# Kernel tuning notes

Measured on AMD Instinct MI355X. Metric: run time of the kernel, lower is better.

## Reference

```python
import jax, jax.numpy as jnp
import numpy as np
import math

D_MODEL = 1024
H = 16
D_K = D_MODEL // H
D_FF = 4096
NEG = -1e9


def layer_norm(x, alpha, bias):
    # Faithful to source: mean over last dim, UNBIASED std (torch.std default),
    # eps defined in source but never used in forward.
    mean = jnp.mean(x, axis=-1, keepdims=True)
    std = jnp.std(x, axis=-1, ddof=1, keepdims=True)
    return (x - mean) / std * alpha + bias


def mha(x, mask, w_q, w_k, w_v, w_o):
    B, S, D = x.shape
    q = (x @ w_q.T).reshape(B, S, H, D_K)
    k = (x @ w_k.T).reshape(B, S, H, D_K)
    v = (x @ w_v.T).reshape(B, S, H, D_K)
    scores = jnp.einsum('bqhd,bkhd->bhqk', q, k) / math.sqrt(D_K)
    scores = jnp.where(mask, NEG, scores)
    attn = jax.nn.softmax(scores, axis=-1)
    out = jnp.einsum('bhqk,bkhd->bqhd', attn, v).reshape(B, S, D)
    return out @ w_o.T


def setup_inputs() -> dict:
    key = jax.random.key(0)
    ks = jax.random.split(key, 16)
    B, S = 4, 2048
    s = 0.02
    return {
        'x': jax.random.normal(ks[0], (B, S, D_MODEL), jnp.float32),
        'w_q': jax.random.normal(ks[1], (D_MODEL, D_MODEL), jnp.float32) * s,
        'w_k': jax.random.normal(ks[2], (D_MODEL, D_MODEL), jnp.float32) * s,
        'w_v': jax.random.normal(ks[3], (D_MODEL, D_MODEL), jnp.float32) * s,
        'w_o': jax.random.normal(ks[4], (D_MODEL, D_MODEL), jnp.float32) * s,
        'l1_w': jax.random.normal(ks[5], (D_FF, D_MODEL), jnp.float32) * s,
        'l1_b': jnp.zeros((D_FF,), jnp.float32),
        'l2_w': jax.random.normal(ks[6], (D_MODEL, D_FF), jnp.float32) * s,
        'l2_b': jnp.zeros((D_MODEL,), jnp.float32),
        'norm1_a': jnp.ones((D_MODEL,), jnp.float32),
        'norm1_b': jnp.zeros((D_MODEL,), jnp.float32),
        'norm2_a': jnp.ones((D_MODEL,), jnp.float32),
        'norm2_b': jnp.zeros((D_MODEL,), jnp.float32),
        'normf_a': jnp.ones((D_MODEL,), jnp.float32),
        'normf_b': jnp.zeros((D_MODEL,), jnp.float32),
        'mask': jax.random.randint(ks[7], (B, 1, 1, S), 0, 2) == 1,
    }


def reference(x, w_q, w_k, w_v, w_o, l1_w, l1_b, l2_w, l2_b,
              norm1_a, norm1_b, norm2_a, norm2_b, normf_a, normf_b, mask):
    # residual 1: pre-norm self-attention (dropout is identity at eval)
    x = x + mha(layer_norm(x, norm1_a, norm1_b), mask, w_q, w_k, w_v, w_o)
    # residual 2: pre-norm FFN
    h = layer_norm(x, norm2_a, norm2_b)
    ff = jax.nn.relu(h @ l1_w.T + l1_b) @ l2_w.T + l2_b
    x = x + ff
    return layer_norm(x, normf_a, normf_b)
```

## Files before the change

kernel.cpp:

```cpp
#include <hip/hip_runtime.h>
#include <hip/hip_bf16.h>


typedef __bf16 bf16x8 __attribute__((ext_vector_type(8)));
typedef float f32x4 __attribute__((ext_vector_type(4)));
typedef unsigned short u16x8 __attribute__((ext_vector_type(8)));
using bf16 = __hip_bfloat16;

__device__ __forceinline__ f32x4 mfma16(bf16x8 a, bf16x8 b, f32x4 c) {
  return __builtin_amdgcn_mfma_f32_16x16x32_bf16(a, b, c, 0, 0, 0);
}

__device__ __forceinline__ int swz(int row, int blk) {
  return row * 64 + ((blk ^ (row & 7)) << 3);
}

__device__ __forceinline__ void stage_tile64(unsigned short* lds,
                                             const bf16* g, int ld, int rows) {
  const int lane = threadIdx.x & 63, wid = threadIdx.x >> 6;
  const int r8 = lane >> 3, blk = lane & 7;
  const bf16* gl = g + (size_t)r8 * ld + ((blk ^ r8) << 3);
  const int passes = rows >> 3;
  for (int p = wid; p < passes; p += 4) {
    __builtin_amdgcn_global_load_lds(
        (const __attribute__((address_space(1))) void*)(gl + (size_t)(p * 8) * ld),
        (__attribute__((address_space(3))) void*)(lds + p * 512),
        16, 0, 0);
  }
}

__device__ __forceinline__ short bfb(float x) {
  return (short)__hip_bfloat16_raw(__float2bfloat16(x)).x;
}

__global__ __launch_bounds__(256) void cvt_k(const float* __restrict__ s,
                                             bf16* __restrict__ d, int n) {
  const int i = (blockIdx.x * 256 + threadIdx.x) * 4;
  if (i + 3 < n) {
    const float4 v = *reinterpret_cast<const float4*>(s + i);
    ushort4 o;
    o.x = (unsigned short)bfb(v.x);
    o.y = (unsigned short)bfb(v.y);
    o.z = (unsigned short)bfb(v.z);
    o.w = (unsigned short)bfb(v.w);
    *reinterpret_cast<ushort4*>(d + i) = o;
  }
}

template <bool OUT_F32>
__global__ __launch_bounds__(256) void layernorm_k(const float* __restrict__ in,
                                                   const float* __restrict__ gamma,
                                                   const float* __restrict__ beta,
                                                   void* __restrict__ out) {
  __shared__ float red[8];
  const int row = blockIdx.x, t = threadIdx.x;
  const float4 vv = reinterpret_cast<const float4*>(in + (size_t)row * 1024)[t];
  const float x0 = vv.x, x1 = vv.y, x2 = vv.z, x3 = vv.w;
  float s = x0 + x1 + x2 + x3;
#pragma unroll
  for (int off = 32; off; off >>= 1) s += __shfl_down(s, off);
  if ((t & 63) == 0) red[t >> 6] = s;
  __syncthreads();
  const float mean = (red[0] + red[1] + red[2] + red[3]) * (1.0f / 1024.0f);
  const float d0 = x0 - mean, d1 = x1 - mean, d2 = x2 - mean, d3 = x3 - mean;
  float sq = d0 * d0 + d1 * d1 + d2 * d2 + d3 * d3;
#pragma unroll
  for (int off = 32; off; off >>= 1) sq += __shfl_down(sq, off);
  if ((t & 63) == 0) red[4 + (t >> 6)] = sq;
  __syncthreads();
  const float var =
      fmaxf((red[4] + red[5] + red[6] + red[7]) * (1.0f / 1023.0f), 1e-20f);
  const float rstd = rsqrtf(var);
  const float4 ga = reinterpret_cast<const float4*>(gamma)[t];
  const float4 be = reinterpret_cast<const float4*>(beta)[t];
  const float y0 = d0 * rstd * ga.x + be.x;
  const float y1 = d1 * rstd * ga.y + be.y;
  const float y2 = d2 * rstd * ga.z + be.z;
  const float y3 = d3 * rstd * ga.w + be.w;
  if (OUT_F32) {
    reinterpret_cast<float4*>((float*)out + (size_t)row * 1024)[t] =
        make_float4(y0, y1, y2, y3);
  } else {
    ushort4 o;
    o.x = (unsigned short)bfb(y0);
    o.y = (unsigned short)bfb(y1);
    o.z = (unsigned short)bfb(y2);
    o.w = (unsigned short)bfb(y3);
    reinterpret_cast<ushort4*>((bf16*)out + (size_t)row * 1024)[t] = o;
  }
}

template <bool HAS_BIAS, bool RELU, bool HAS_RES, bool OUT_F32, bool KV_EXIT>
__global__ __launch_bounds__(256) void gemm_bt(const bf16* __restrict__ A,
                                               const bf16* __restrict__ W,
                                               const float* __restrict__ bias,
                                               const float* __restrict__ resid,
                                               void* __restrict__ out,
                                               int M, int N, int K,
                                               int lda, int ldw,
                                               const int* __restrict__ cnt) {
  __shared__ __align__(16) unsigned short As[128 * 64];
  __shared__ __align__(16) unsigned short Bs[128 * 64];
  int bx = blockIdx.x, by = blockIdx.y;
  const int nwg = gridDim.x * gridDim.y;
  if ((nwg & 7) == 0) {
    const int lid = by * gridDim.x + bx;
    const int cpx = nwg >> 3;
    const int s = (lid & 7) * cpx + (lid >> 3);
    bx = s % gridDim.x;
    by = s / gridDim.x;
  }
  const int tm = bx * 128, tn = by * 128;
  if (KV_EXIT) {
    const int npad = (cnt[tm >> 11] + 127) & ~127;
    if ((tm & 2047) >= npad) return;
  }
  const int lane = threadIdx.x & 63, wid = threadIdx.x >> 6;
  const int n16 = lane & 15, quad = lane >> 4;
  const int wm = (wid >> 1) * 64, wn = (wid & 1) * 64;
  f32x4 acc[4][4] = {};
  for (int k0 = 0; k0 < K; k0 += 64) {
    stage_tile64(As, A + (size_t)tm * lda + k0, lda, 128);
    stage_tile64(Bs, W + (size_t)tn * ldw + k0, ldw, 128);
    __syncthreads();
#pragma unroll
    for (int kk = 0; kk < 64; kk += 32) {
      bf16x8 af[4], bw[4];
#pragma unroll
      for (int i = 0; i < 4; ++i)
        af[i] = *reinterpret_cast<const bf16x8*>(
            &As[swz(wm + i * 16 + n16, (kk >> 3) + quad)]);
#pragma unroll
      for (int j = 0; j < 4; ++j)
        bw[j] = *reinterpret_cast<const bf16x8*>(
            &Bs[swz(wn + j * 16 + n16, (kk >> 3) + quad)]);
#pragma unroll
      for (int i = 0; i < 4; ++i)
#pragma unroll
        for (int j = 0; j < 4; ++j) acc[i][j] = mfma16(af[i], bw[j], acc[i][j]);
    }
    __syncthreads();
  }
#pragma unroll
  for (int i = 0; i < 4; ++i) {
#pragma unroll
    for (int j = 0; j < 4; ++j) {
      const int n = tn + wn + j * 16 + n16;
      const float bv = HAS_BIAS ? bias[n] : 0.0f;
#pragma unroll
      for (int r = 0; r < 4; ++r) {
        const int m = tm + wm + i * 16 + quad * 4 + r;
        float vv = acc[i][j][r] + bv;
        if (RELU) vv = fmaxf(vv, 0.0f);
        if (HAS_RES) vv += resid[(size_t)m * N + n];
        if (OUT_F32)
          ((float*)out)[(size_t)m * N + n] = vv;
        else
          ((bf16*)out)[(size_t)m * N + n] = __float2bfloat16(vv);
      }
    }
  }
}

__global__ __launch_bounds__(256) void prep_mask_k(const int* __restrict__ m,
                                                   float* __restrict__ mf,
                                                   int n) {
  __shared__ int s;
  if (threadIdx.x == 0) s = 0;
  __syncthreads();
  unsigned int acc = 0;
  for (int i = threadIdx.x; i < 512; i += 256)
    acc |= ((const unsigned int*)m)[i] & 0xFFFFFF00u;
  if (acc) atomicOr(&s, 1);
  __syncthreads();
  const bool bytes = (s != 0);
  const int i = blockIdx.x * 256 + threadIdx.x;
  if (i < n) {
    const int v = bytes ? (int)((const unsigned char*)m)[i] : m[i];
    mf[i] = v ? -1.4427e9f : 0.0f;
  }
}

__global__ __launch_bounds__(256) void scan_k(const float* __restrict__ maskf,
                                              float* __restrict__ cmask,
                                              int* __restrict__ idx,
                                              int* __restrict__ cnt) {
  __shared__ int wsum[4];
  const int b = blockIdx.x, t = threadIdx.x, lane = t & 63, w = t >> 6;
  const float* mrow = maskf + b * 2048;
  int keep[8], local = 0;
#pragma unroll
  for (int e = 0; e < 8; ++e) {
    keep[e] = (mrow[t * 8 + e] == 0.0f) ? 1 : 0;
    local += keep[e];
  }
  int inc = local;
#pragma unroll
  for (int off = 1; off < 64; off <<= 1) {
    int v = __shfl_up(inc, off);
    if (lane >= off) inc += v;
  }
  if (lane == 63) wsum[w] = inc;
  __syncthreads();
  int base = 0;
#pragma unroll
  for (int i = 0; i < 4; ++i)
    if (i < w) base += wsum[i];
  int p = base + inc - local;
#pragma unroll
  for (int e = 0; e < 8; ++e)
    if (keep[e]) idx[b * 2048 + p++] = t * 8 + e;
  const int total = wsum[0] + wsum[1] + wsum[2] + wsum[3];
  if (t == 0) cnt[b] = total;
  for (int i = t; i < 2048; i += 256)
    cmask[b * 2048 + i] = (i < total) ? 0.0f : -1.4427e9f;
}

__global__ __launch_bounds__(128) void gatherA_k(const bf16* __restrict__ ln1,
                                                 const int* __restrict__ idx,
                                                 const int* __restrict__ cnt,
                                                 bf16* __restrict__ cln) {
  const int b = blockIdx.x >> 11, j = blockIdx.x & 2047;
  const int n = cnt[b];
  const int npad = (n + 127) & ~127;
  if (j >= npad) return;
  u16x8* dst = reinterpret_cast<u16x8*>(cln + ((size_t)(b * 2048 + j)) * 1024);
  if (j < n) {
    const int s = idx[b * 2048 + j];
    const u16x8* src =
        reinterpret_cast<const u16x8*>(ln1 + ((size_t)(b * 2048 + s)) * 1024);
    dst[threadIdx.x] = src[threadIdx.x];
  } else {
    u16x8 z = {};
    dst[threadIdx.x] = z;
  }
}

__global__ __launch_bounds__(256) void attn_k(const bf16* __restrict__ q,
                                              const bf16* __restrict__ kv,
                                              const float* __restrict__ cmask,
                                              const int* __restrict__ cnt,
                                              bf16* __restrict__ out, int BHN) {
  __shared__ __align__(16) unsigned short Ks[2][64 * 64];
  __shared__ __align__(16) unsigned short Vs[2][64 * 72];
  const int lane = threadIdx.x & 63, wid = threadIdx.x >> 6;
  const int n16 = lane & 15, quad = lane >> 4;
  const int bid = blockIdx.x;
  const int bh = bid % BHN, qb = bid / BHN;
  const int b = bh >> 4, h = bh & 15;
  const bf16* qp0 = q + (size_t)b * 2048 * 1024 + h * 64;
  const bf16* kp0 = kv + (size_t)b * 2048 * 2048 + h * 64;
  const bf16* vp0 = kp0 + 1024;
  const float* mfb = cmask + b * 2048;
  const int cntb = cnt[b];
  const int nk = ((cntb + 63) >> 6) << 6;
  const int qrow0 = qb * 128 + wid * 32;

  bf16x8 qf[2][2];
#pragma unroll
  for (int g = 0; g < 2; ++g) {
    const bf16* qp = qp0 + (size_t)(qrow0 + g * 16 + n16) * 1024 + quad * 8;
    qf[g][0] = *reinterpret_cast<const bf16x8*>(qp);
    qf[g][1] = *reinterpret_cast<const bf16x8*>(qp + 32);
  }
  bf16x8 ones;
#pragma unroll
  for (int e = 0; e < 8; ++e) ones[e] = (__bf16)1.0f;
  f32x4 oacc[2][4] = {};
  f32x4 lacc[2] = {};
  const int prow = ((n16 >> 2) << 3) + (n16 & 3);
  const int vkey = lane, vdc = wid * 16;

  stage_tile64(Ks[0], kp0, 2048, 64);
  {
    const bf16* vp = vp0 + (size_t)vkey * 2048 + vdc;
    const u16x8 a = *reinterpret_cast<const u16x8*>(vp);
    const u16x8 bq = *reinterpret_cast<const u16x8*>(vp + 8);
#pragma unroll
    for (int e = 0; e < 8; ++e) {
      Vs[0][(vdc + e) * 72 + vkey] = a[e];
      Vs[0][(vdc + 8 + e) * 72 + vkey] = bq[e];
    }
  }
  int cur = 0;
  for (int kt = 0; kt < nk; kt += 64) {
    __syncthreads();
    const bool hasNext = (kt + 64 < nk);
    const bool fullTile = (kt + 64 <= cntb);
    u16x8 na = {}, nb = {};
    if (hasNext) {
      stage_tile64(Ks[cur ^ 1], kp0 + (size_t)(kt + 64) * 2048, 2048, 64);
      const bf16* vp = vp0 + (size_t)(kt + 64 + vkey) * 2048 + vdc;
      na = *reinterpret_cast<const u16x8*>(vp);
      nb = *reinterpret_cast<const u16x8*>(vp + 8);
    }
    const unsigned short* Kc = Ks[cur];
    const unsigned short* Vc = Vs[cur];
#pragma unroll
    for (int sub = 0; sub < 2; ++sub) {
      const int kb = sub * 32;
      bf16x8 aflo[2], afhi[2];
#pragma unroll
      for (int st = 0; st < 2; ++st) {
        const int row = kb + prow + st * 4;
        aflo[st] = *reinterpret_cast<const bf16x8*>(&Kc[swz(row, quad)]);
        afhi[st] = *reinterpret_cast<const bf16x8*>(&Kc[swz(row, 4 + quad)]);
      }
      __builtin_amdgcn_s_setprio(1);
      f32x4 z[2][2];
#pragma unroll
      for (int g = 0; g < 2; ++g)
#pragma unroll
        for (int st = 0; st < 2; ++st) {
          f32x4 zz = {};
          zz = mfma16(aflo[st], qf[g][0], zz);
          zz = mfma16(afhi[st], qf[g][1], zz);
          z[g][st] = zz;
        }
      __builtin_amdgcn_s_setprio(0);
      float4 m0 = make_float4(0.f, 0.f, 0.f, 0.f);
      float4 m1 = make_float4(0.f, 0.f, 0.f, 0.f);
      if (!fullTile) {
        m0 = *reinterpret_cast<const float4*>(mfb + kt + kb + quad * 8);
        m1 = *reinterpret_cast<const float4*>(mfb + kt + kb + quad * 8 + 4);
      }
      bf16x8 vf[4];
#pragma unroll
      for (int j = 0; j < 4; ++j)
        vf[j] = *reinterpret_cast<const bf16x8*>(
            &Vc[(j * 16 + n16) * 72 + kb + quad * 8]);
#pragma unroll
      for (int g = 0; g < 2; ++g) {
        bf16x8 pf;
#pragma unroll
        for (int r = 0; r < 4; ++r) {
          const float e0 = __builtin_amdgcn_exp2f(
              fmaf(z[g][0][r], 0.18033688f, ((const float*)&m0)[r]));
          const float e1 = __builtin_amdgcn_exp2f(
              fmaf(z[g][1][r], 0.18033688f, ((const float*)&m1)[r]));
          pf[r] = (__bf16)e0;
          pf[4 + r] = (__bf16)e1;
        }
        __builtin_amdgcn_s_setprio(1);
#pragma unroll
        for (int j = 0; j < 4; ++j) oacc[g][j] = mfma16(pf, vf[j], oacc[g][j]);
        lacc[g] = mfma16(pf, ones, lacc[g]);
        __builtin_amdgcn_s_setprio(0);
      }
    }
    if (hasNext) {
      unsigned short* Vn = Vs[cur ^ 1];
#pragma unroll
      for (int e = 0; e < 8; ++e) {
        Vn[(vdc + e) * 72 + vkey] = na[e];
        Vn[(vdc + 8 + e) * 72 + vkey] = nb[e];
      }
    }
    cur ^= 1;
  }
#pragma unroll
  for (int g = 0; g < 2; ++g) {
#pragma unroll
    for (int r = 0; r < 4; ++r) {
      const float lr = 1.0f / fmaxf(lacc[g][r], 1e-20f);
      bf16* op =
          out + (size_t)(b * 2048 + qrow0 + g * 16 + quad * 4 + r) * 1024 +
          h * 64;
#pragma unroll
      for (int j = 0; j < 4; ++j)
        op[j * 16 + n16] = __float2bfloat16(oacc[g][j][r] * lr);
    }
  }
}

extern "C" void kernel_launch(void* const* d_in, const int* in_sizes, int n_in,
                              void* d_out, int out_size, void* d_ws,
                              size_t ws_size, hipStream_t stream) {
  const float* x    = (const float*)d_in[0];
  const float* w_q  = (const float*)d_in[1];
  const float* w_k  = (const float*)d_in[2];
  const float* w_v  = (const float*)d_in[3];
  const float* w_o  = (const float*)d_in[4];
  const float* l1_w = (const float*)d_in[5];
  const float* l1_b = (const float*)d_in[6];
  const float* l2_w = (const float*)d_in[7];
  const float* l2_b = (const float*)d_in[8];
  const float* n1a  = (const float*)d_in[9];
  const float* n1b  = (const float*)d_in[10];
  const float* n2a  = (const float*)d_in[11];
  const float* n2b  = (const float*)d_in[12];
  const float* nfa  = (const float*)d_in[13];
  const float* nfb  = (const float*)d_in[14];
  const int* mask   = (const int*)d_in[15];

  const int D = 1024, FF = 4096;
  const int M = in_sizes[0] / D;
  const int B = M / 2048;

  const size_t MB = 1024ull * 1024ull;
  if (ws_size < 121 * MB) return;
  char* w = (char*)d_ws;
  bf16* WQKV = (bf16*)(w + 0 * MB);
  bf16* WO   = (bf16*)(w + 6 * MB);
  bf16* L1W  = (bf16*)(w + 8 * MB);
  bf16* L2W  = (bf16*)(w + 16 * MB);
  bf16* LN1  = (bf16*)(w + 24 * MB);
  bf16* Qbuf = (bf16*)(w + 40 * MB);
  bf16* ATT  = LN1;
  bf16* HLN  = (bf16*)(w + 40 * MB);
  bf16* CLN  = (bf16*)(w + 56 * MB);
  bf16* FF1  = (bf16*)(w + 56 * MB);
  bf16* KV   = (bf16*)(w + 88 * MB);
  float* X1  = (float*)(w + 88 * MB);
  float* MASKF = (float*)(w + 120 * MB);
  float* CMASK = (float*)(w + 120 * MB + 256 * 1024);
  int*   IDX   = (int*)(w + 120 * MB + 512 * 1024);
  int*   CNT   = (int*)(w + 120 * MB + 768 * 1024);

  const dim3 blk(256);
  cvt_k<<<dim3(D * D / 1024), blk, 0, stream>>>(w_q, WQKV, D * D);
  cvt_k<<<dim3(D * D / 1024), blk, 0, stream>>>(w_k, WQKV + D * D, D * D);
  cvt_k<<<dim3(D * D / 1024), blk, 0, stream>>>(w_v, WQKV + 2 * D * D, D * D);
  cvt_k<<<dim3(D * D / 1024), blk, 0, stream>>>(w_o, WO, D * D);
  cvt_k<<<dim3(FF * D / 1024), blk, 0, stream>>>(l1_w, L1W, FF * D);
  cvt_k<<<dim3(FF * D / 1024), blk, 0, stream>>>(l2_w, L2W, FF * D);
  prep_mask_k<<<dim3((M + 255) / 256), blk, 0, stream>>>(mask, MASKF, M);
  scan_k<<<dim3(B), blk, 0, stream>>>(MASKF, CMASK, IDX, CNT);

  layernorm_k<false><<<M, blk, 0, stream>>>(x, n1a, n1b, LN1);
  gemm_bt<false, false, false, false, false>
      <<<dim3(M / 128, D / 128), blk, 0, stream>>>(LN1, WQKV, nullptr, nullptr,
                                                   Qbuf, M, D, D, D, D,
                                                   nullptr);
  gatherA_k<<<dim3(B * 2048), dim3(128), 0, stream>>>(LN1, IDX, CNT, CLN);
  gemm_bt<false, false, false, false, true>
      <<<dim3(M / 128, 2048 / 128), blk, 0, stream>>>(
          CLN, WQKV + (size_t)D * D, nullptr, nullptr, KV, M, 2048, D, D, D,
          CNT);
  const int BHN = B * 16;
  attn_k<<<dim3((M / 128) * 16), blk, 0, stream>>>(Qbuf, KV, CMASK, CNT, ATT,
                                                   BHN);
  gemm_bt<false, false, true, true, false>
      <<<dim3(M / 128, D / 128), blk, 0, stream>>>(ATT, WO, nullptr, x, X1, M,
                                                   D, D, D, D, nullptr);
  layernorm_k<false><<<M, blk, 0, stream>>>(X1, n2a, n2b, HLN);
  for (int c = 0; c < 2; ++c) {
    gemm_bt<true, true, false, false, false>
        <<<dim3(M / 128, 2048 / 128), blk, 0, stream>>>(
            HLN, L1W + (size_t)c * 2048 * D, l1_b + c * 2048, nullptr, FF1, M,
            2048, D, D, D, nullptr);
    if (c == 0)
      gemm_bt<true, false, true, true, false>
          <<<dim3(M / 128, D / 128), blk, 0, stream>>>(
              FF1, L2W + c * 2048, l2_b, X1, X1, M, D, 2048, 2048, FF,
              nullptr);
    else
      gemm_bt<false, false, true, true, false>
          <<<dim3(M / 128, D / 128), blk, 0, stream>>>(
              FF1, L2W + c * 2048, nullptr, X1, X1, M, D, 2048, 2048, FF,
              nullptr);
  }
  layernorm_k<true><<<M, blk, 0, stream>>>(X1, nfa, nfb, (float*)d_out);
}
```

Baseline: 538.7 us.

## Fuse Q and compacted KV projections into one GEMM launch; drop tile swizzle

The separate Q projection GEMM and the compacted K/V projection GEMM are merged into one dedicated kernel with a 24-column grid. The first 8 column tiles compute Q from the full layernorm output and the rest compute K/V from the gathered rows, with early exit for padded rows. This removes one launch and lets Q and KV tiles share the GPU at the same time. The generic GEMM also loses its XCD-aware block remapping, which may reduce L2 locality for the remaining GEMMs.

```diff
diff --git a/kernel.cpp b/kernel.cpp
--- a/kernel.cpp
+++ b/kernel.cpp
@@ -90,34 +90,20 @@
   }
 }
 
-template <bool HAS_BIAS, bool RELU, bool HAS_RES, bool OUT_F32, bool KV_EXIT>
+template <bool HAS_BIAS, bool RELU, bool HAS_RES, bool OUT_F32>
 __global__ __launch_bounds__(256) void gemm_bt(const bf16* __restrict__ A,
                                                const bf16* __restrict__ W,
                                                const float* __restrict__ bias,
                                                const float* __restrict__ resid,
                                                void* __restrict__ out,
                                                int M, int N, int K,
-                                               int lda, int ldw,
-                                               const int* __restrict__ cnt) {
+                                               int lda, int ldw) {
   __shared__ __align__(16) unsigned short As[128 * 64];
   __shared__ __align__(16) unsigned short Bs[128 * 64];
-  int bx = blockIdx.x, by = blockIdx.y;
-  const int nwg = gridDim.x * gridDim.y;
-  if ((nwg & 7) == 0) {
-    const int lid = by * gridDim.x + bx;
-    const int cpx = nwg >> 3;
-    const int s = (lid & 7) * cpx + (lid >> 3);
-    bx = s % gridDim.x;
-    by = s / gridDim.x;
-  }
-  const int tm = bx * 128, tn = by * 128;
-  if (KV_EXIT) {
-    const int npad = (cnt[tm >> 11] + 127) & ~127;
-    if ((tm & 2047) >= npad) return;
-  }
   const int lane = threadIdx.x & 63, wid = threadIdx.x >> 6;
   const int n16 = lane & 15, quad = lane >> 4;
   const int wm = (wid >> 1) * 64, wn = (wid & 1) * 64;
+  const int tm = blockIdx.x * 128, tn = blockIdx.y * 128;
   f32x4 acc[4][4] = {};
   for (int k0 = 0; k0 < K; k0 += 64) {
     stage_tile64(As, A + (size_t)tm * lda + k0, lda, 128);
@@ -157,6 +143,65 @@
           ((float*)out)[(size_t)m * N + n] = vv;
         else
           ((bf16*)out)[(size_t)m * N + n] = __float2bfloat16(vv);
+      }
+    }
+  }
+}
+
+__global__ __launch_bounds__(256) void gemm_qkv_k(const bf16* __restrict__ ln1,
+                                                  const bf16* __restrict__ cln,
+                                                  const bf16* __restrict__ wqkv,
+                                                  const int* __restrict__ cnt,
+                                                  bf16* __restrict__ qout,
+                                                  bf16* __restrict__ kvout) {
+  __shared__ __align__(16) unsigned short As[128 * 64];
+  __shared__ __align__(16) unsigned short Bs[128 * 64];
+  const int tm = blockIdx.x * 128, by = blockIdx.y;
+  const bool isQ = (by < 8);
+  if (!isQ) {
+    const int npad = (cnt[tm >> 11] + 127) & ~127;
+    if ((tm & 2047) >= npad) return;
+  }
+  const bf16* Ap = isQ ? ln1 : cln;
+  const int tn = by * 128;
+  const int lane = threadIdx.x & 63, wid = threadIdx.x >> 6;
+  const int n16 = lane & 15, quad = lane >> 4;
+  const int wm = (wid >> 1) * 64, wn = (wid & 1) * 64;
+  f32x4 acc[4][4] = {};
+  for (int k0 = 0; k0 < 1024; k0 += 64) {
+    stage_tile64(As, Ap + (size_t)tm * 1024 + k0, 1024, 128);
+    stage_tile64(Bs, wqkv + (size_t)tn * 1024 + k0, 1024, 128);
+    __syncthreads();
+#pragma unroll
+    for (int kk = 0; kk < 64; kk += 32) {
+      bf16x8 af[4], bw[4];
+#pragma unroll
+      for (int i = 0; i < 4; ++i)
+        af[i] = *reinterpret_cast<const bf16x8*>(
+            &As[swz(wm + i * 16 + n16, (kk >> 3) + quad)]);
+#pragma unroll
+      for (int j = 0; j < 4; ++j)
+        bw[j] = *reinterpret_cast<const bf16x8*>(
+            &Bs[swz(wn + j * 16 + n16, (kk >> 3) + quad)]);
+#pragma unroll
+      for (int i = 0; i < 4; ++i)
+#pragma unroll
+        for (int j = 0; j < 4; ++j) acc[i][j] = mfma16(af[i], bw[j], acc[i][j]);
+    }
+    __syncthreads();
+  }
+  bf16* outp = isQ ? qout : kvout;
+  const int ldo = isQ ? 1024 : 2048;
+  const int nc0 = isQ ? tn : tn - 1024;
+#pragma unroll
+  for (int i = 0; i < 4; ++i) {
+#pragma unroll
+    for (int j = 0; j < 4; ++j) {
+      const int n = nc0 + wn + j * 16 + n16;
+#pragma unroll
+      for (int r = 0; r < 4; ++r) {
+        const int m = tm + wm + i * 16 + quad * 4 + r;
+        outp[(size_t)m * ldo + n] = __float2bfloat16(acc[i][j][r]);
       }
     }
   }
@@ -428,37 +473,28 @@
   scan_k<<<dim3(B), blk, 0, stream>>>(MASKF, CMASK, IDX, CNT);
 
   layernorm_k<false><<<M, blk, 0, stream>>>(x, n1a, n1b, LN1);
-  gemm_bt<false, false, false, false, false>
-      <<<dim3(M / 128, D / 128), blk, 0, stream>>>(LN1, WQKV, nullptr, nullptr,
-                                                   Qbuf, M, D, D, D, D,
-                                                   nullptr);
   gatherA_k<<<dim3(B * 2048), dim3(128), 0, stream>>>(LN1, IDX, CNT, CLN);
-  gemm_bt<false, false, false, false, true>
-      <<<dim3(M / 128, 2048 / 128), blk, 0, stream>>>(
-          CLN, WQKV + (size_t)D * D, nullptr, nullptr, KV, M, 2048, D, D, D,
-          CNT);
+  gemm_qkv_k<<<dim3(M / 128, 24), blk, 0, stream>>>(LN1, CLN, WQKV, CNT, Qbuf,
+                                                    KV);
   const int BHN = B * 16;
   attn_k<<<dim3((M / 128) * 16), blk, 0, stream>>>(Qbuf, KV, CMASK, CNT, ATT,
                                                    BHN);
-  gemm_bt<false, false, true, true, false>
-      <<<dim3(M / 128, D / 128), blk, 0, stream>>>(ATT, WO, nullptr, x, X1, M,
-                                                   D, D, D, D, nullptr);
+  gemm_bt<false, false, true, true><<<dim3(M / 128, D / 128), blk, 0, stream>>>(
+      ATT, WO, nullptr, x, X1, M, D, D, D, D);
   layernorm_k<false><<<M, blk, 0, stream>>>(X1, n2a, n2b, HLN);
   for (int c = 0; c < 2; ++c) {
-    gemm_bt<true, true, false, false, false>
+    gemm_bt<true, true, false, false>
         <<<dim3(M / 128, 2048 / 128), blk, 0, stream>>>(
             HLN, L1W + (size_t)c * 2048 * D, l1_b + c * 2048, nullptr, FF1, M,
-            2048, D, D, D, nullptr);
+            2048, D, D, D);
     if (c == 0)
-      gemm_bt<true, false, true, true, false>
+      gemm_bt<true, false, true, true>
           <<<dim3(M / 128, D / 128), blk, 0, stream>>>(
-              FF1, L2W + c * 2048, l2_b, X1, X1, M, D, 2048, 2048, FF,
-              nullptr);
+              FF1, L2W + c * 2048, l2_b, X1, X1, M, D, 2048, 2048, FF);
     else
-      gemm_bt<false, false, true, true, false>
+      gemm_bt<false, false, true, true>
           <<<dim3(M / 128, D / 128), blk, 0, stream>>>(
-              FF1, L2W + c * 2048, nullptr, X1, X1, M, D, 2048, 2048, FF,
-              nullptr);
+              FF1, L2W + c * 2048, nullptr, X1, X1, M, D, 2048, 2048, FF);
   }
   layernorm_k<true><<<M, blk, 0, stream>>>(X1, nfa, nfb, (float*)d_out);
 }
```

Result: faster. 518.0 us (-3.9%).
